# Optimization experiments

Measured on AMD Instinct MI355X. Metric: run time of the kernel, lower is better.

The kernel has to match this reference:

```python
import jax, jax.numpy as jnp
import numpy as np

B, S, D = 4, 2048, 1024
E, K = 8, 2
H = 4 * D  # expert hidden (expansion=4)


def setup_inputs() -> dict:
    key = jax.random.key(0)
    ks = jax.random.split(key, 5)
    x = jax.random.normal(ks[0], (B, S, D), dtype=jnp.float32)
    Wr = jax.random.normal(ks[1], (E, D), dtype=jnp.float32) * 0.02
    br = jnp.zeros((E,), dtype=jnp.float32)
    W1 = jax.random.normal(ks[2], (E, H, D), dtype=jnp.float32) * 0.02
    b1 = jnp.zeros((E, H), dtype=jnp.float32)
    W2 = jax.random.normal(ks[3], (E, D, H), dtype=jnp.float32) * 0.02
    b2 = jnp.zeros((E, D), dtype=jnp.float32)
    return {"x": x, "Wr": Wr, "br": br, "W1": W1, "b1": b1, "W2": W2, "b2": b2}


def reference(x, Wr, br, W1, b1, W2, b2):
    # Dropout is inactive (eval mode). torch Linear: y = x @ W.T + b.
    Bb, Ss, Dm = x.shape
    xf = x.reshape(-1, Dm)                       # [T, D], T = B*S
    logits = xf @ Wr.T + br                      # [T, E]
    probs = jax.nn.softmax(logits, axis=-1)      # [T, E]
    topw, topi = jax.lax.top_k(probs, K)         # [T, K]
    topw = topw / jnp.sum(topw, axis=-1, keepdims=True)
    # combine weights per (token, expert): sum over k slots of renormalized weight
    comb = jnp.sum(jax.nn.one_hot(topi, E, dtype=xf.dtype) * topw[..., None], axis=1)  # [T, E]
    # dense per-expert MLP over all tokens, then weighted combine
    h = jax.nn.gelu(jnp.einsum('td,ehd->eth', xf, W1) + b1[:, None, :], approximate=False)  # [E, T, 4D]
    oe = jnp.einsum('eth,edh->etd', h, W2) + b2[:, None, :]                                  # [E, T, D]
    out = jnp.einsum('te,etd->td', comb, oe)     # [T, D]
    return out.reshape(Bb, Ss, Dm)
```

## Files before the change

### kernel.cpp

```cpp
#include <hip/hip_runtime.h>

#define T_TOK 8192
#define DMODEL 1024
#define NEXP 8
#define TOPK 2
#define HID 4096
#define NPAIR (T_TOK*TOPK)
#define BM 128
#define BN 128
#define BK 64
#define MAXT (NPAIR/128 + NEXP)

typedef unsigned short u16;
typedef unsigned int u32;
typedef short s16x8 __attribute__((ext_vector_type(8)));
typedef float f32x4 __attribute__((ext_vector_type(4)));

__device__ __forceinline__ u16 f2b(float f) {
    union { float f; unsigned int u; } v; v.f = f;
    return (u16)((v.u + 0x7fffu + ((v.u >> 16) & 1u)) >> 16);
}
__device__ __forceinline__ float b2f(u16 h) {
    union { unsigned int u; float f; } v; v.u = ((unsigned int)h) << 16;
    return v.f;
}

__device__ __forceinline__ s16x8 cvt8(float4 f0, float4 f1) {
    s16x8 o;
    o[0]=(short)f2b(f0.x); o[1]=(short)f2b(f0.y); o[2]=(short)f2b(f0.z); o[3]=(short)f2b(f0.w);
    o[4]=(short)f2b(f1.x); o[5]=(short)f2b(f1.y); o[6]=(short)f2b(f1.z); o[7]=(short)f2b(f1.w);
    return o;
}

__device__ __forceinline__ void gload16(const void* g, void* l) {
    __builtin_amdgcn_global_load_lds(
        (const __attribute__((address_space(1))) unsigned int*)g,
        (__attribute__((address_space(3))) unsigned int*)l, 16, 0, 0);
}

__device__ __forceinline__ float gelu_fast(float v) {
    float y = 0.7978845608028654f * v * fmaf(0.044715f * v, v, 1.0f);
    float t = -2.8853900817779268f * y;
    float z, r;
    asm("v_exp_f32 %0, %1" : "=v"(z) : "v"(t));
    float den = 1.0f + z;
    asm("v_rcp_f32 %0, %1" : "=v"(r) : "v"(den));
    return v * r;
}

__device__ __forceinline__ int xcd_swz(int bid, int nact) {
    int q = nact >> 3, r = nact & 7;
    int xcd = bid & 7, i = bid >> 3;
    return (xcd < r ? xcd * (q + 1) : r * (q + 1) + (xcd - r) * q) + i;
}

__global__ __launch_bounds__(256) void cvt_kernel(const float* __restrict__ in,
                                                  u16* __restrict__ out, long n8) {
    long stride = (long)gridDim.x * 256;
    for (long i = (long)blockIdx.x * 256 + threadIdx.x; i < n8; i += stride) {
        const float4* p = (const float4*)(in + i * 8);
        float4 f0 = p[0], f1 = p[1];
        *(s16x8*)(out + i * 8) = cvt8(f0, f1);
    }
}

__global__ __launch_bounds__(256) void router_kernel(
    const float* __restrict__ x, const float* __restrict__ Wr, const float* __restrict__ br,
    int* __restrict__ topi, float* __restrict__ topw,
    const float* __restrict__ W1, u16* __restrict__ W1b)
{
    __shared__ float WrS[NEXP * DMODEL];
    int tid = threadIdx.x;
    const float4* Wr4 = (const float4*)Wr;
    float4* WrS4 = (float4*)WrS;
    for (int i = tid; i < NEXP * DMODEL / 4; i += 256) WrS4[i] = Wr4[i];
    __syncthreads();

    int wid = tid >> 6, lane = tid & 63;
    int t = blockIdx.x * 4 + wid;
    const float* xr = x + (size_t)t * DMODEL;

    float acc[NEXP];
#pragma unroll
    for (int e = 0; e < NEXP; ++e) acc[e] = 0.f;
#pragma unroll 4
    for (int i = lane; i < DMODEL; i += 64) {
        float xv = xr[i];
#pragma unroll
        for (int e = 0; e < NEXP; ++e) acc[e] = fmaf(xv, WrS[e * DMODEL + i], acc[e]);
    }
#pragma unroll
    for (int e = 0; e < NEXP; ++e) {
        float v = acc[e];
#pragma unroll
        for (int off = 32; off > 0; off >>= 1) v += __shfl_xor(v, off);
        acc[e] = v;
    }
    if (lane == 0) {
        float lg[NEXP];
#pragma unroll
        for (int e = 0; e < NEXP; ++e) lg[e] = acc[e] + br[e];
        int i1 = 0;
#pragma unroll
        for (int e = 1; e < NEXP; ++e) if (lg[e] > lg[i1]) i1 = e;
        int i2 = (i1 == 0) ? 1 : 0;
#pragma unroll
        for (int e = 0; e < NEXP; ++e) if (e != i1 && lg[e] > lg[i2]) i2 = e;
        float e2 = expf(lg[i2] - lg[i1]);
        float s = 1.f + e2;
        topi[t * 2] = i1;  topi[t * 2 + 1] = i2;
        topw[t * 2] = 1.f / s;  topw[t * 2 + 1] = e2 / s;
    }

    long n8 = (long)NEXP * DMODEL * HID / 8;
    long stride = (long)gridDim.x * 256;
    for (long i = (long)blockIdx.x * 256 + tid; i < n8; i += stride) {
        const float4* p = (const float4*)(W1 + i * 8);
        float4 f0 = p[0], f1 = p[1];
        *(s16x8*)(W1b + i * 8) = cvt8(f0, f1);
    }
}

__global__ __launch_bounds__(256) void count_offsets_kernel(
    const int* __restrict__ topi, int* __restrict__ cnt, int* __restrict__ offs,
    u32* __restrict__ table, int* __restrict__ meta)
{
    __shared__ int red[NEXP * 256];
    int tid = threadIdx.x;
    int c[NEXP] = {};
    for (int i = tid; i < NPAIR; i += 256) {
        int e = topi[i];
#pragma unroll
        for (int k = 0; k < NEXP; ++k) c[k] += (e == k) ? 1 : 0;
    }
#pragma unroll
    for (int k = 0; k < NEXP; ++k) red[k * 256 + tid] = c[k];
    __syncthreads();
    if (tid < NEXP) {
        int s = 0;
        for (int i = 0; i < 256; ++i) s += red[tid * 256 + i];
        cnt[tid] = s;
    }
    __syncthreads();
    if (tid == 0) {
        int a = 0;
        for (int e = 0; e < NEXP; ++e) { offs[e] = a; a += cnt[e]; }
        offs[NEXP] = a;
        int nt = 0;
        for (int e = 0; e < NEXP; ++e)
            for (int r0 = 0; r0 < cnt[e]; r0 += 128)
                table[nt++] = ((u32)e << 20) | (u32)r0;
        meta[0] = nt;
    }
}

__global__ __launch_bounds__(256) void scatter_kernel(
    const int* __restrict__ topi, const float* __restrict__ topw,
    const int* __restrict__ offs, int* __restrict__ fill,
    int* __restrict__ tok, float* __restrict__ wgt, int* __restrict__ pos)
{
    int t = blockIdx.x * 256 + threadIdx.x;
    int lane = threadIdx.x & 63;
#pragma unroll
    for (int s = 0; s < TOPK; ++s) {
        int e = topi[t * 2 + s];
        float w = topw[t * 2 + s];
#pragma unroll
        for (int ex = 0; ex < NEXP; ++ex) {
            unsigned long long m = __ballot(e == ex);
            if (e == ex) {
                int ldr = (int)__ffsll((unsigned long long)m) - 1;
                int base = 0;
                if (lane == ldr) base = atomicAdd(&fill[ex * 32], (int)__popcll(m));
                base = __shfl(base, ldr);
                int mypos = base + (int)__popcll(m & ((1ull << lane) - 1ull));
                int p = offs[ex] + mypos;
                tok[p] = t;
                wgt[p] = w;
                pos[t * 2 + s] = p;
            }
        }
    }
}

__global__ __launch_bounds__(256) void combine_kernel(
    const u16* __restrict__ Op, const int* __restrict__ pos, float* __restrict__ out)
{
    const size_t PL = (size_t)NPAIR * DMODEL;
    int tid = threadIdx.x;
    int t = blockIdx.x * 2 + (tid >> 7);
    int c = (tid & 127) * 8;
    int pa = pos[t * 2], pb = pos[t * 2 + 1];
    s16x8 a0 = *(const s16x8*)(Op + (size_t)pa * DMODEL + c);
    s16x8 a1 = *(const s16x8*)(Op + PL + (size_t)pa * DMODEL + c);
    s16x8 b0 = *(const s16x8*)(Op + (size_t)pb * DMODEL + c);
    s16x8 b1 = *(const s16x8*)(Op + PL + (size_t)pb * DMODEL + c);
    float* o = out + (size_t)t * DMODEL + c;
    float4 o0, o1;
    o0.x = (b2f((u16)a0[0]) + b2f((u16)a1[0])) + (b2f((u16)b0[0]) + b2f((u16)b1[0]));
    o0.y = (b2f((u16)a0[1]) + b2f((u16)a1[1])) + (b2f((u16)b0[1]) + b2f((u16)b1[1]));
    o0.z = (b2f((u16)a0[2]) + b2f((u16)a1[2])) + (b2f((u16)b0[2]) + b2f((u16)b1[2]));
    o0.w = (b2f((u16)a0[3]) + b2f((u16)a1[3])) + (b2f((u16)b0[3]) + b2f((u16)b1[3]));
    o1.x = (b2f((u16)a0[4]) + b2f((u16)a1[4])) + (b2f((u16)b0[4]) + b2f((u16)b1[4]));
    o1.y = (b2f((u16)a0[5]) + b2f((u16)a1[5])) + (b2f((u16)b0[5]) + b2f((u16)b1[5]));
    o1.z = (b2f((u16)a0[6]) + b2f((u16)a1[6])) + (b2f((u16)b0[6]) + b2f((u16)b1[6]));
    o1.w = (b2f((u16)a0[7]) + b2f((u16)a1[7])) + (b2f((u16)b0[7]) + b2f((u16)b1[7]));
    ((float4*)o)[0] = o0;
    ((float4*)o)[1] = o1;
}

#define STAGE_TILE(koff) do {                                               \
    _Pragma("unroll") for (int c = 0; c < 4; ++c) {                         \
        int idx = c * 256 + tid;                                            \
        gload16(Agp + aoffA[c] + (size_t)(koff), (char*)As + idx * 16);     \
        gload16(Bgp + boffB[c] + (size_t)(koff), (char*)Bs + idx * 16);     \
    }                                                                       \
} while (0)

#define COMPUTE_TILE() do {                                                 \
    _Pragma("unroll") for (int half = 0; half < 2; ++half) {                \
        s16x8 av[4], bv[4];                                                 \
        int kslot = half * 4 + (lane >> 4);                                 \
        _Pragma("unroll") for (int mi = 0; mi < 4; ++mi) {                  \
            int rr = wm * 64 + mi * 16 + (lane & 15);                       \
            av[mi] = *(const s16x8*)((char*)As + rr * 128 + ((kslot ^ (rr & 7)) * 16)); } \
        _Pragma("unroll") for (int nf = 0; nf < 4; ++nf) {                  \
            int rb = wn * 64 + nf * 16 + (lane & 15);                       \
            bv[nf] = *(const s16x8*)((char*)Bs + rb * 128 + ((kslot ^ (rb & 7)) * 16)); } \
        _Pragma("unroll") for (int mi = 0; mi < 4; ++mi)                    \
        _Pragma("unroll") for (int nf = 0; nf < 4; ++nf)                    \
            acc[mi][nf] = __builtin_amdgcn_mfma_f32_16x16x32_bf16(          \
                av[mi], bv[nf], acc[mi][nf], 0, 0, 0);                      \
    }                                                                       \
} while (0)

#define VM0() asm volatile("s_waitcnt vmcnt(0)" ::: "memory")

#define M97_LOOP(NT, KBASE) do {                                            \
    _Pragma("unroll 1")                                                     \
    for (int t = 0; t < (NT); ++t) {                                        \
        STAGE_TILE((size_t)(KBASE) + (size_t)t * BK);                       \
        VM0();                                                              \
        __syncthreads();                                                    \
        COMPUTE_TILE();                                                     \
        __syncthreads();                                                    \
    }                                                                       \
} while (0)

#define CHUNK_RS(c)                                                         \
    int r##c = ((c) * 256 + tid) >> 3;                                      \
    int s##c = (tid & 7) ^ (r##c & 7);

__global__ __launch_bounds__(256, 3) void gemm1_kernel(
    const u16* __restrict__ xb, const u16* __restrict__ W1b, const float* __restrict__ b1,
    const int* __restrict__ tok, const int* __restrict__ cnt, const int* __restrict__ offs,
    const u32* __restrict__ table, const int* __restrict__ meta,
    u16* __restrict__ H1, int p0, int p1,
    const float* __restrict__ W2, u16* __restrict__ W2b)
{
    __shared__ __align__(16) u16 As[BM * BK];
    __shared__ __align__(16) u16 Bs[BN * BK];
    const int tid = threadIdx.x;
    const int lane = tid & 63, wid = tid >> 6;
    const int wm = wid >> 1, wn = wid & 1;

    const int NCOL = HID / BN;
    int nt = meta[0];
    int nact = NCOL * nt;
    int bid = blockIdx.x;
    bool active = (bid < nact);
    int e = 0, row0 = 0, ce = 0, oe = 0, col0 = 0;
    if (active) {
        int swz = xcd_swz(bid, nact);
        int tile = swz / NCOL, colb = swz & (NCOL - 1);
        u32 entry = table[tile];
        e = (int)(entry >> 20);
        row0 = (int)(entry & 0xFFFFFu);
        ce = cnt[e]; oe = offs[e];
        col0 = colb * BN;
        active = !(oe + min(ce, row0 + BM) <= p0 || oe + row0 >= p1);
    }

    if (active) {
        f32x4 acc[4][4] = {};
        const u16* Agp = xb;
        const u16* Bgp = W1b;
        size_t aoffA[4], boffB[4];
        {
            CHUNK_RS(0) CHUNK_RS(1) CHUNK_RS(2) CHUNK_RS(3)
#define TOKA(rc) ((row0 + (rc)) < ce ? tok[oe + row0 + (rc)] : tok[oe])
            aoffA[0] = (size_t)TOKA(r0) * DMODEL + s0 * 8;
            aoffA[1] = (size_t)TOKA(r1) * DMODEL + s1 * 8;
            aoffA[2] = (size_t)TOKA(r2) * DMODEL + s2 * 8;
            aoffA[3] = (size_t)TOKA(r3) * DMODEL + s3 * 8;
#undef TOKA
            boffB[0] = ((size_t)e * HID + col0 + r0) * DMODEL + s0 * 8;
            boffB[1] = ((size_t)e * HID + col0 + r1) * DMODEL + s1 * 8;
            boffB[2] = ((size_t)e * HID + col0 + r2) * DMODEL + s2 * 8;
            boffB[3] = ((size_t)e * HID + col0 + r3) * DMODEL + s3 * 8;
        }

        M97_LOOP(DMODEL / BK, 0);

        float bias[4];
#pragma unroll
        for (int nf = 0; nf < 4; ++nf)
            bias[nf] = b1[e * HID + col0 + wn * 64 + nf * 16 + (lane & 15)];

#pragma unroll
        for (int mf = 0; mf < 4; ++mf) {
#pragma unroll
            for (int j = 0; j < 4; ++j) {
                int r = wm * 64 + mf * 16 + ((lane >> 4) * 4) + j;
                int gi = row0 + r;
                int p = oe + gi;
                if (gi < ce && p >= p0 && p < p1) {
                    u16* hrow = H1 + (size_t)(p - p0) * HID;
#pragma unroll
                    for (int nf = 0; nf < 4; ++nf) {
                        int n = col0 + wn * 64 + nf * 16 + (lane & 15);
                        hrow[n] = f2b(gelu_fast(acc[mf][nf][j] + bias[nf]));
                    }
                }
            }
        }
    }

    if (p0 == 0) {
        long n8 = (long)NEXP * DMODEL * HID / 8;
        long stride = (long)gridDim.x * 256;
        for (long i = (long)bid * 256 + tid; i < n8; i += stride) {
            const float4* p = (const float4*)(W2 + i * 8);
            float4 f0 = p[0], f1 = p[1];
            *(s16x8*)(W2b + i * 8) = cvt8(f0, f1);
        }
    }
}

__global__ __launch_bounds__(256, 3) void gemm2_kernel(
    const u16* __restrict__ H1, const u16* __restrict__ W2b, const float* __restrict__ b2,
    const float* __restrict__ wgt,
    const int* __restrict__ cnt, const int* __restrict__ offs,
    const u32* __restrict__ table, const int* __restrict__ meta,
    u16* __restrict__ Opair, int p0, int p1)
{
    __shared__ __align__(16) u16 As[BM * BK];
    __shared__ __align__(16) u16 Bs[BN * BK];
    const int tid = threadIdx.x;
    const int lane = tid & 63, wid = tid >> 6;
    const int wm = wid >> 1, wn = wid & 1;

    int nt = meta[0];
    int nact = 16 * nt;
    int bid = blockIdx.x;
    if (bid >= nact) return;
    int swz = xcd_swz(bid, nact);
    int tile = swz >> 4;
    int rem = swz & 15;
    int colb = rem >> 1, khalf = rem & 1;
    u32 entry = table[tile];
    const int e = (int)(entry >> 20);
    const int row0 = (int)(entry & 0xFFFFFu);
    const int ce = cnt[e], oe = offs[e];
    if (oe + min(ce, row0 + BM) <= p0 || oe + row0 >= p1) return;
    const int col0 = colb * BN;
    const int kbase = khalf * (HID / 2);

    f32x4 acc[4][4] = {};

    const u16* Agp = H1;
    const u16* Bgp = W2b;
    const int smax = p1 - p0 - 1;
    size_t aoffA[4], boffB[4];
    {
        CHUNK_RS(0) CHUNK_RS(1) CHUNK_RS(2) CHUNK_RS(3)
#define AIDX(rc) ({ int ai_ = oe + row0 + (rc) - p0;                         \
                    ai_ < 0 ? 0 : (ai_ > smax ? smax : ai_); })
        aoffA[0] = (size_t)AIDX(r0) * HID + s0 * 8 + kbase;
        aoffA[1] = (size_t)AIDX(r1) * HID + s1 * 8 + kbase;
        aoffA[2] = (size_t)AIDX(r2) * HID + s2 * 8 + kbase;
        aoffA[3] = (size_t)AIDX(r3) * HID + s3 * 8 + kbase;
#undef AIDX
        boffB[0] = ((size_t)e * DMODEL + col0 + r0) * HID + s0 * 8 + kbase;
        boffB[1] = ((size_t)e * DMODEL + col0 + r1) * HID + s1 * 8 + kbase;
        boffB[2] = ((size_t)e * DMODEL + col0 + r2) * HID + s2 * 8 + kbase;
        boffB[3] = ((size_t)e * DMODEL + col0 + r3) * HID + s3 * 8 + kbase;
    }

    M97_LOOP(HID / 2 / BK, 0);

    float bias[4];
#pragma unroll
    for (int nf = 0; nf < 4; ++nf)
        bias[nf] = (khalf == 0)
            ? b2[e * DMODEL + col0 + wn * 64 + nf * 16 + (lane & 15)] : 0.0f;

    u16* Opl = Opair + (size_t)khalf * NPAIR * DMODEL;
#pragma unroll
    for (int mf = 0; mf < 4; ++mf) {
#pragma unroll
        for (int j = 0; j < 4; ++j) {
            int r = wm * 64 + mf * 16 + ((lane >> 4) * 4) + j;
            int gi = row0 + r;
            int p = oe + gi;
            if (gi < ce && p >= p0 && p < p1) {
                float w = wgt[p];
                u16* orow = Opl + (size_t)p * DMODEL;
#pragma unroll
                for (int nf = 0; nf < 4; ++nf) {
                    int n = col0 + wn * 64 + nf * 16 + (lane & 15);
                    orow[n] = f2b(w * (acc[mf][nf][j] + bias[nf]));
                }
            }
        }
    }
}

extern "C" void kernel_launch(void* const* d_in, const int* in_sizes, int n_in,
                              void* d_out, int out_size, void* d_ws, size_t ws_size,
                              hipStream_t stream)
{
    const float* x  = (const float*)d_in[0];
    const float* Wr = (const float*)d_in[1];
    const float* br = (const float*)d_in[2];
    const float* W1 = (const float*)d_in[3];
    const float* b1 = (const float*)d_in[4];
    const float* W2 = (const float*)d_in[5];
    const float* b2 = (const float*)d_in[6];
    float* out = (float*)d_out;

    char* ws = (char*)d_ws;
    u16* xb = (u16*)ws;
    size_t o2 = (size_t)T_TOK * DMODEL * 2;
    int*   cnt   = (int*)(ws + o2);
    int*   offs  = (int*)(ws + o2 + 64);
    int*   meta  = (int*)(ws + o2 + 192);
    u32*   table = (u32*)(ws + o2 + 256);
    int*   fill  = (int*)(ws + o2 + 1024);
    int*   topi  = (int*)(ws + o2 + 4096);
    float* topw  = (float*)(ws + o2 + 4096 + (size_t)NPAIR * 4);
    int*   tok   = (int*)(ws + o2 + 4096 + (size_t)NPAIR * 8);
    float* wgt   = (float*)(ws + o2 + 4096 + (size_t)NPAIR * 12);
    int*   pos   = (int*)(ws + o2 + 4096 + (size_t)NPAIR * 16);

    const size_t WBYTES = (size_t)NEXP * DMODEL * HID * 2;
    size_t oW2 = o2 + (2u << 20);
    size_t oW1 = oW2 + WBYTES;
    size_t oOp = oW1 + WBYTES;
    size_t oH  = oOp + (size_t)2 * NPAIR * DMODEL * 2;
    u16* W2b   = (u16*)(ws + oW2);
    u16* W1b   = (u16*)(ws + oW1);
    u16* Opair = (u16*)(ws + oOp);
    u16* H1    = (u16*)(ws + oH);

    long long cap = ((long long)ws_size - (long long)oH) / ((long long)HID * 2);
    int slice = cap >= NPAIR ? NPAIR : (cap < 1024 ? 1024 : (int)cap);

    hipMemsetAsync(ws + o2, 0, 2048, stream);

    cvt_kernel<<<dim3(1024), 256, 0, stream>>>(x, xb, (long)T_TOK * DMODEL / 8);

    router_kernel<<<dim3(T_TOK / 4), 256, 0, stream>>>(x, Wr, br, topi, topw, W1, W1b);
    count_offsets_kernel<<<dim3(1), 256, 0, stream>>>(topi, cnt, offs, table, meta);
    scatter_kernel<<<dim3(T_TOK / 256), 256, 0, stream>>>(topi, topw, offs, fill, tok, wgt, pos);

    for (int pp = 0; pp < NPAIR; pp += slice) {
        int p1v = pp + slice < NPAIR ? pp + slice : NPAIR;
        gemm1_kernel<<<dim3((HID / BN) * MAXT), 256, 0, stream>>>(
            xb, W1b, b1, tok, cnt, offs, table, meta, H1, pp, p1v, W2, W2b);
        gemm2_kernel<<<dim3(16 * MAXT), 256, 0, stream>>>(
            H1, W2b, b2, wgt, cnt, offs, table, meta, Opair, pp, p1v);
    }

    combine_kernel<<<dim3(T_TOK / 2), 256, 0, stream>>>(Opair, pos, out);
}
```

Measured before the change: 489.9 us.

## Drop split-K in expert down-projection and fold x conversion into router

The second expert GEMM now runs the full hidden dimension in one block instead of splitting K into two halves written to separate partial-output planes. The combine kernel therefore reads one bf16 plane per pair instead of two, which halves the intermediate write/read traffic and drops a rounding step. Separately, the standalone fp32-to-bf16 conversion of x is merged into the router kernel to save a launch. The tradeoff is half as many GEMM2 blocks, each with twice the K loop, so occupancy and tail behaviour across the CUs change.

```diff
diff --git a/kernel.cpp b/kernel.cpp
--- a/kernel.cpp
+++ b/kernel.cpp
@@ -54,20 +54,10 @@
     return (xcd < r ? xcd * (q + 1) : r * (q + 1) + (xcd - r) * q) + i;
 }
 
-__global__ __launch_bounds__(256) void cvt_kernel(const float* __restrict__ in,
-                                                  u16* __restrict__ out, long n8) {
-    long stride = (long)gridDim.x * 256;
-    for (long i = (long)blockIdx.x * 256 + threadIdx.x; i < n8; i += stride) {
-        const float4* p = (const float4*)(in + i * 8);
-        float4 f0 = p[0], f1 = p[1];
-        *(s16x8*)(out + i * 8) = cvt8(f0, f1);
-    }
-}
-
 __global__ __launch_bounds__(256) void router_kernel(
     const float* __restrict__ x, const float* __restrict__ Wr, const float* __restrict__ br,
     int* __restrict__ topi, float* __restrict__ topw,
-    const float* __restrict__ W1, u16* __restrict__ W1b)
+    u16* __restrict__ xb, const float* __restrict__ W1, u16* __restrict__ W1b)
 {
     __shared__ float WrS[NEXP * DMODEL];
     int tid = threadIdx.x;
@@ -110,6 +100,16 @@
         float s = 1.f + e2;
         topi[t * 2] = i1;  topi[t * 2 + 1] = i2;
         topw[t * 2] = 1.f / s;  topw[t * 2 + 1] = e2 / s;
+    }
+
+    {
+        const float* xblk = x + (size_t)blockIdx.x * 4 * DMODEL;
+        u16* xbblk = xb + (size_t)blockIdx.x * 4 * DMODEL;
+#pragma unroll
+        for (int i = tid; i < 4 * DMODEL / 8; i += 256) {
+            const float4* p = (const float4*)(xblk + i * 8);
+            *(s16x8*)(xbblk + i * 8) = cvt8(p[0], p[1]);
+        }
     }
 
     long n8 = (long)NEXP * DMODEL * HID / 8;
@@ -186,25 +186,22 @@
 __global__ __launch_bounds__(256) void combine_kernel(
     const u16* __restrict__ Op, const int* __restrict__ pos, float* __restrict__ out)
 {
-    const size_t PL = (size_t)NPAIR * DMODEL;
     int tid = threadIdx.x;
     int t = blockIdx.x * 2 + (tid >> 7);
     int c = (tid & 127) * 8;
     int pa = pos[t * 2], pb = pos[t * 2 + 1];
-    s16x8 a0 = *(const s16x8*)(Op + (size_t)pa * DMODEL + c);
-    s16x8 a1 = *(const s16x8*)(Op + PL + (size_t)pa * DMODEL + c);
-    s16x8 b0 = *(const s16x8*)(Op + (size_t)pb * DMODEL + c);
-    s16x8 b1 = *(const s16x8*)(Op + PL + (size_t)pb * DMODEL + c);
+    s16x8 a = *(const s16x8*)(Op + (size_t)pa * DMODEL + c);
+    s16x8 b = *(const s16x8*)(Op + (size_t)pb * DMODEL + c);
     float* o = out + (size_t)t * DMODEL + c;
     float4 o0, o1;
-    o0.x = (b2f((u16)a0[0]) + b2f((u16)a1[0])) + (b2f((u16)b0[0]) + b2f((u16)b1[0]));
-    o0.y = (b2f((u16)a0[1]) + b2f((u16)a1[1])) + (b2f((u16)b0[1]) + b2f((u16)b1[1]));
-    o0.z = (b2f((u16)a0[2]) + b2f((u16)a1[2])) + (b2f((u16)b0[2]) + b2f((u16)b1[2]));
-    o0.w = (b2f((u16)a0[3]) + b2f((u16)a1[3])) + (b2f((u16)b0[3]) + b2f((u16)b1[3]));
-    o1.x = (b2f((u16)a0[4]) + b2f((u16)a1[4])) + (b2f((u16)b0[4]) + b2f((u16)b1[4]));
-    o1.y = (b2f((u16)a0[5]) + b2f((u16)a1[5])) + (b2f((u16)b0[5]) + b2f((u16)b1[5]));
-    o1.z = (b2f((u16)a0[6]) + b2f((u16)a1[6])) + (b2f((u16)b0[6]) + b2f((u16)b1[6]));
-    o1.w = (b2f((u16)a0[7]) + b2f((u16)a1[7])) + (b2f((u16)b0[7]) + b2f((u16)b1[7]));
+    o0.x = b2f((u16)a[0]) + b2f((u16)b[0]);
+    o0.y = b2f((u16)a[1]) + b2f((u16)b[1]);
+    o0.z = b2f((u16)a[2]) + b2f((u16)b[2]);
+    o0.w = b2f((u16)a[3]) + b2f((u16)b[3]);
+    o1.x = b2f((u16)a[4]) + b2f((u16)b[4]);
+    o1.y = b2f((u16)a[5]) + b2f((u16)b[5]);
+    o1.z = b2f((u16)a[6]) + b2f((u16)b[6]);
+    o1.w = b2f((u16)a[7]) + b2f((u16)b[7]);
     ((float4*)o)[0] = o0;
     ((float4*)o)[1] = o1;
 }
@@ -350,21 +347,19 @@
     const int lane = tid & 63, wid = tid >> 6;
     const int wm = wid >> 1, wn = wid & 1;
 
+    const int NCOL = DMODEL / BN;
     int nt = meta[0];
-    int nact = 16 * nt;
+    int nact = NCOL * nt;
     int bid = blockIdx.x;
     if (bid >= nact) return;
     int swz = xcd_swz(bid, nact);
-    int tile = swz >> 4;
-    int rem = swz & 15;
-    int colb = rem >> 1, khalf = rem & 1;
+    int tile = swz >> 3, colb = swz & 7;
     u32 entry = table[tile];
     const int e = (int)(entry >> 20);
     const int row0 = (int)(entry & 0xFFFFFu);
     const int ce = cnt[e], oe = offs[e];
     if (oe + min(ce, row0 + BM) <= p0 || oe + row0 >= p1) return;
     const int col0 = colb * BN;
-    const int kbase = khalf * (HID / 2);
 
     f32x4 acc[4][4] = {};
 
@@ -376,26 +371,24 @@
         CHUNK_RS(0) CHUNK_RS(1) CHUNK_RS(2) CHUNK_RS(3)
 #define AIDX(rc) ({ int ai_ = oe + row0 + (rc) - p0;                         \
                     ai_ < 0 ? 0 : (ai_ > smax ? smax : ai_); })
-        aoffA[0] = (size_t)AIDX(r0) * HID + s0 * 8 + kbase;
-        aoffA[1] = (size_t)AIDX(r1) * HID + s1 * 8 + kbase;
-        aoffA[2] = (size_t)AIDX(r2) * HID + s2 * 8 + kbase;
-        aoffA[3] = (size_t)AIDX(r3) * HID + s3 * 8 + kbase;
+        aoffA[0] = (size_t)AIDX(r0) * HID + s0 * 8;
+        aoffA[1] = (size_t)AIDX(r1) * HID + s1 * 8;
+        aoffA[2] = (size_t)AIDX(r2) * HID + s2 * 8;
+        aoffA[3] = (size_t)AIDX(r3) * HID + s3 * 8;
 #undef AIDX
-        boffB[0] = ((size_t)e * DMODEL + col0 + r0) * HID + s0 * 8 + kbase;
-        boffB[1] = ((size_t)e * DMODEL + col0 + r1) * HID + s1 * 8 + kbase;
-        boffB[2] = ((size_t)e * DMODEL + col0 + r2) * HID + s2 * 8 + kbase;
-        boffB[3] = ((size_t)e * DMODEL + col0 + r3) * HID + s3 * 8 + kbase;
-    }
-
-    M97_LOOP(HID / 2 / BK, 0);
+        boffB[0] = ((size_t)e * DMODEL + col0 + r0) * HID + s0 * 8;
+        boffB[1] = ((size_t)e * DMODEL + col0 + r1) * HID + s1 * 8;
+        boffB[2] = ((size_t)e * DMODEL + col0 + r2) * HID + s2 * 8;
+        boffB[3] = ((size_t)e * DMODEL + col0 + r3) * HID + s3 * 8;
+    }
+
+    M97_LOOP(HID / BK, 0);
 
     float bias[4];
 #pragma unroll
     for (int nf = 0; nf < 4; ++nf)
-        bias[nf] = (khalf == 0)
-            ? b2[e * DMODEL + col0 + wn * 64 + nf * 16 + (lane & 15)] : 0.0f;
-
-    u16* Opl = Opair + (size_t)khalf * NPAIR * DMODEL;
+        bias[nf] = b2[e * DMODEL + col0 + wn * 64 + nf * 16 + (lane & 15)];
+
 #pragma unroll
     for (int mf = 0; mf < 4; ++mf) {
 #pragma unroll
@@ -405,7 +398,7 @@
             int p = oe + gi;
             if (gi < ce && p >= p0 && p < p1) {
                 float w = wgt[p];
-                u16* orow = Opl + (size_t)p * DMODEL;
+                u16* orow = Opair + (size_t)p * DMODEL;
 #pragma unroll
                 for (int nf = 0; nf < 4; ++nf) {
                     int n = col0 + wn * 64 + nf * 16 + (lane & 15);
@@ -447,7 +440,7 @@
     size_t oW2 = o2 + (2u << 20);
     size_t oW1 = oW2 + WBYTES;
     size_t oOp = oW1 + WBYTES;
-    size_t oH  = oOp + (size_t)2 * NPAIR * DMODEL * 2;
+    size_t oH  = oOp + (size_t)NPAIR * DMODEL * 2;
     u16* W2b   = (u16*)(ws + oW2);
     u16* W1b   = (u16*)(ws + oW1);
     u16* Opair = (u16*)(ws + oOp);
@@ -458,9 +451,7 @@
 
     hipMemsetAsync(ws + o2, 0, 2048, stream);
 
-    cvt_kernel<<<dim3(1024), 256, 0, stream>>>(x, xb, (long)T_TOK * DMODEL / 8);
-
-    router_kernel<<<dim3(T_TOK / 4), 256, 0, stream>>>(x, Wr, br, topi, topw, W1, W1b);
+    router_kernel<<<dim3(T_TOK / 4), 256, 0, stream>>>(x, Wr, br, topi, topw, xb, W1, W1b);
     count_offsets_kernel<<<dim3(1), 256, 0, stream>>>(topi, cnt, offs, table, meta);
     scatter_kernel<<<dim3(T_TOK / 256), 256, 0, stream>>>(topi, topw, offs, fill, tok, wgt, pos);
 
@@ -468,7 +459,7 @@
         int p1v = pp + slice < NPAIR ? pp + slice : NPAIR;
         gemm1_kernel<<<dim3((HID / BN) * MAXT), 256, 0, stream>>>(
             xb, W1b, b1, tok, cnt, offs, table, meta, H1, pp, p1v, W2, W2b);
-        gemm2_kernel<<<dim3(16 * MAXT), 256, 0, stream>>>(
+        gemm2_kernel<<<dim3((DMODEL / BN) * MAXT), 256, 0, stream>>>(
             H1, W2b, b2, wgt, cnt, offs, table, meta, Opair, pp, p1v);
     }
 
```

Result: no change. 495.1 us (+1.1%).
